# Performance work log

Hardware: AMD Instinct MI355X
Metric: run time of the kernel (lower is better)

## Reference

```python
import jax, jax.numpy as jnp
import numpy as np

B, T, INPUT_DIM = 32, 256, 512
VQ_DIM = 128
NUM_EMBED = 8192
CODEBOOK_NUM = 1
SPLIT_NUM = 4
FREQ = INPUT_DIM // 2 + 1  # 257


def setup_inputs() -> dict:
    key = jax.random.key(0)
    k1, k2, k3, k4 = jax.random.split(key, 4)
    x = jax.random.normal(k1, (B, T, INPUT_DIM), dtype=jnp.float32)
    # xavier_normal_ on (input_dim, vq_dim): std = sqrt(2/(fan_in+fan_out))
    xav_std = float(np.sqrt(2.0 / (INPUT_DIM + VQ_DIM)))
    projector = jax.random.normal(k2, (INPUT_DIM, VQ_DIM), dtype=jnp.float32) * xav_std
    codebook = jax.random.normal(k3, (CODEBOOK_NUM, NUM_EMBED, VQ_DIM), dtype=jnp.float32)
    random_matrix = jax.random.randint(k4, (FREQ,), 0, SPLIT_NUM, dtype=jnp.int32)
    return {"x": x, "projector": projector, "codebook": codebook,
            "random_matrix": random_matrix}


def reference(x, projector, codebook, random_matrix):
    n = x.shape[-1]
    x_fft = jnp.fft.rfft(x, axis=-1)                              # [B,T,F] complex
    # masks[s, f] = (random_matrix[f] == s); vectorizes the per-split list
    masks = (random_matrix[None, :] == jnp.arange(SPLIT_NUM)[:, None])  # [S,F] bool
    x_sub = x_fft[:, :, None, :] * masks                           # [B,T,S,F]
    x_recon = jnp.fft.irfft(x_sub, n=n, axis=-1)                   # [B,T,S,n]
    feat = jnp.einsum('btns,sd->btnd', x_recon, projector)         # [B,T,S,D]
    feat = feat / jnp.linalg.norm(feat, axis=-1, keepdims=True)
    cb = codebook / jnp.linalg.norm(codebook, axis=-1, keepdims=True)  # [C,M,D]
    sim = jnp.einsum('btnd,cmd->btncm', feat, cb)                  # [B,T,S,C,M]
    return jnp.argmax(sim, axis=-1)                                # [B,T,S,C]
```

## Files before the change

kernel.cpp:

```cpp
#include <hip/hip_runtime.h>
#include <math.h>

#define BT 8192
#define NDIM 512
#define NFREQ 257
#define DDIM 128
#define NEMBED 8192
#define NQ 4
#define ROWS 32768

typedef _Float16 half8 __attribute__((ext_vector_type(8)));
typedef float f32x4 __attribute__((ext_vector_type(4)));

#define SCALE_DN 2.44140625e-4f

__global__ __launch_bounds__(256) void prep_kernel(const float* __restrict__ cb,
                                                   const float* __restrict__ proj,
                                                   const int* __restrict__ rm,
                                                   _Float16* __restrict__ chi,
                                                   _Float16* __restrict__ clo,
                                                   _Float16* __restrict__ Wth,
                                                   _Float16* __restrict__ Wtl) {
    int t = threadIdx.x;
    if (blockIdx.x < 512) {
        __shared__ float tile[16][132];
        __shared__ float rns[16];
        int tileIdx = blockIdx.x;
        int row = t >> 4, seg = t & 15;
        const float* src = cb + ((size_t)tileIdx * 16 + row) * DDIM + seg * 8;
        float4 v0 = *(const float4*)src;
        float4 v1 = *(const float4*)(src + 4);
        *(float4*)&tile[row][seg * 8] = v0;
        *(float4*)&tile[row][seg * 8 + 4] = v1;
        float ss = v0.x * v0.x;
        ss = fmaf(v0.y, v0.y, ss); ss = fmaf(v0.z, v0.z, ss); ss = fmaf(v0.w, v0.w, ss);
        ss = fmaf(v1.x, v1.x, ss); ss = fmaf(v1.y, v1.y, ss);
        ss = fmaf(v1.z, v1.z, ss); ss = fmaf(v1.w, v1.w, ss);
#pragma unroll
        for (int m = 1; m < 16; m <<= 1) ss += __shfl_xor(ss, m);
        if (seg == 0) rns[row] = 1.0f / sqrtf(ss);
        __syncthreads();
        int cr = t & 15, lgq = (t >> 4) & 3, kt = t >> 6;
        int k0 = kt * 32 + lgq * 8;
        float rn = rns[cr];
        half8 oh, ol;
#pragma unroll
        for (int j = 0; j < 8; ++j) {
            float f = tile[cr][k0 + j] * rn;
            _Float16 h = (_Float16)f;
            oh[j] = h;
            ol[j] = (_Float16)((f - (float)h) * 4096.0f);
        }
        size_t dst = (size_t)tileIdx * 2048 + t * 8;
        *(half8*)(chi + dst) = oh;
        *(half8*)(clo + dst) = ol;
    } else {
        __shared__ float ctab[512];
        __shared__ float Ks[512];
        __shared__ int rms[NFREQ];
        int bxp = blockIdx.x - 512;
        int s = bxp & 3, ntp = bxp >> 2;
        int d = t & 127;
        int n0 = ntp * 16 + (t >> 7) * 8;
        for (int i = t; i < 512; i += 256) ctab[i] = cospif((float)i * (1.0f / 256.0f));
        for (int i = t; i < NFREQ; i += 256) rms[i] = rm[i];
        __syncthreads();
        for (int base = t; base < 512; base += 256) {
            float acc = 0.0f;
            for (int f = 0; f < NFREQ; ++f) {
                float w = (f == 0 || f == 256) ? 1.0f : 2.0f;
                float c = w * ctab[(f * base) & 511];
                acc += (rms[f] == s) ? c : 0.0f;
            }
            Ks[base] = acc * (1.0f / 512.0f);
        }
        __syncthreads();
        float acc[8] = {};
        for (int p16 = 0; p16 < 512; p16 += 16) {
            float wv[23];
#pragma unroll
            for (int j2 = 0; j2 < 23; ++j2) wv[j2] = Ks[(p16 - n0 + j2 - 7) & 511];
#pragma unroll
            for (int j = 0; j < 16; ++j) {
                float xp = proj[(p16 + j) * DDIM + d];
#pragma unroll
                for (int i = 0; i < 8; ++i)
                    acc[i] = fmaf(xp, wv[7 + j - i], acc[i]);
            }
        }
        size_t cbase = (size_t)(s * DDIM + d) * 512 + n0;
#pragma unroll
        for (int i = 0; i < 8; ++i) {
            float f = acc[i] * 256.0f;
            _Float16 h = (_Float16)f;
            Wth[cbase + i] = h;
            Wtl[cbase + i] = (_Float16)((f - (float)h) * 4096.0f);
        }
    }
}

__global__ __launch_bounds__(256) void fused_feat(const float* __restrict__ x,
                                                  const _Float16* __restrict__ Wth,
                                                  const _Float16* __restrict__ Wtl,
                                                  _Float16* __restrict__ fhi,
                                                  _Float16* __restrict__ flo) {
    __shared__ __align__(16) char smem[59392];
    float* xs = (float*)smem;
    _Float16* Wh = (_Float16*)(smem + 18432);
    _Float16* Wl = (_Float16*)(smem + 38912);

    int t = threadIdx.x;
    int w = t >> 6, lr = t & 15, lg = (t >> 4) & 3;
    int row0 = blockIdx.x * 64;
    int sIdx = blockIdx.y;

    int xr_r = t >> 2, xr_c = (t & 3) * 8;
    int wcol = t >> 1, wh_h = t & 1;
    const float* xsrc = x + (size_t)(row0 + xr_r) * NDIM + xr_c;
    const _Float16* whsrc = Wth + (size_t)(sIdx * 128 + wcol) * 512 + wh_h * 16;
    const _Float16* wlsrc = Wtl + (size_t)(sIdx * 128 + wcol) * 512 + wh_h * 16;

    f32x4 c0[8], c1[8];
#pragma unroll
    for (int i = 0; i < 8; ++i) { c0[i] = (f32x4){0.f,0.f,0.f,0.f}; c1[i] = c0[i]; }

    {
        float4 a0 = *(const float4*)(xsrc);
        float4 a1 = *(const float4*)(xsrc + 4);
        *(float4*)&xs[xr_r * 36 + xr_c] = a0;
        *(float4*)&xs[xr_r * 36 + xr_c + 4] = a1;
        half8 h0 = *(const half8*)(whsrc);
        half8 h1 = *(const half8*)(whsrc + 8);
        half8 l0 = *(const half8*)(wlsrc);
        half8 l1 = *(const half8*)(wlsrc + 8);
        *(half8*)&Wh[wcol * 40 + wh_h * 16] = h0;
        *(half8*)&Wh[wcol * 40 + wh_h * 16 + 8] = h1;
        *(half8*)&Wl[wcol * 40 + wh_h * 16] = l0;
        *(half8*)&Wl[wcol * 40 + wh_h * 16 + 8] = l1;
    }

    for (int it = 0; it < 16; ++it) {
        __syncthreads();
        int buf = it & 1;
        float4 nx0, nx1; half8 nh0, nh1, nl0, nl1;
        bool have = (it + 1) < 16;
        if (have) {
            int k0 = (it + 1) * 32;
            nx0 = *(const float4*)(xsrc + k0);
            nx1 = *(const float4*)(xsrc + k0 + 4);
            nh0 = *(const half8*)(whsrc + k0);
            nh1 = *(const half8*)(whsrc + k0 + 8);
            nl0 = *(const half8*)(wlsrc + k0);
            nl1 = *(const half8*)(wlsrc + k0 + 8);
        }
        const float* xb = xs + buf * 2304;
        float4 f0 = *(const float4*)&xb[(w * 16 + lr) * 36 + lg * 8];
        float4 f1 = *(const float4*)&xb[(w * 16 + lr) * 36 + lg * 8 + 4];
        float fv[8] = {f0.x, f0.y, f0.z, f0.w, f1.x, f1.y, f1.z, f1.w};
        half8 ah, al;
#pragma unroll
        for (int j = 0; j < 8; ++j) {
            _Float16 h = (_Float16)fv[j];
            ah[j] = h;
            al[j] = (_Float16)((fv[j] - (float)h) * 4096.0f);
        }
        const _Float16* whb = Wh + buf * 5120;
        const _Float16* wlb = Wl + buf * 5120;
#pragma unroll
        for (int set = 0; set < 8; ++set) {
            int bcol = set * 16 + lr;
            half8 bh = *(const half8*)&whb[bcol * 40 + lg * 8];
            half8 bl = *(const half8*)&wlb[bcol * 40 + lg * 8];
            c0[set] = __builtin_amdgcn_mfma_f32_16x16x32_f16(ah, bh, c0[set], 0, 0, 0);
            c1[set] = __builtin_amdgcn_mfma_f32_16x16x32_f16(ah, bl, c1[set], 0, 0, 0);
            c1[set] = __builtin_amdgcn_mfma_f32_16x16x32_f16(al, bh, c1[set], 0, 0, 0);
        }
        __syncthreads();
        if (have) {
            *(float4*)&xs[(buf ^ 1) * 2304 + xr_r * 36 + xr_c] = nx0;
            *(float4*)&xs[(buf ^ 1) * 2304 + xr_r * 36 + xr_c + 4] = nx1;
            _Float16* dh = Wh + (buf ^ 1) * 5120 + wcol * 40 + wh_h * 16;
            _Float16* dl = Wl + (buf ^ 1) * 5120 + wcol * 40 + wh_h * 16;
            *(half8*)(dh) = nh0; *(half8*)(dh + 8) = nh1;
            *(half8*)(dl) = nl0; *(half8*)(dl + 8) = nl1;
        }
    }
    __syncthreads();

    float* few = (float*)smem + w * 2112;
    float ss[4] = {0.f, 0.f, 0.f, 0.f};
    float vv[8][4];
#pragma unroll
    for (int set = 0; set < 8; ++set)
#pragma unroll
        for (int r = 0; r < 4; ++r) {
            float v = fmaf(c1[set][r], SCALE_DN, c0[set][r]);
            vv[set][r] = v;
            ss[r] = fmaf(v, v, ss[r]);
        }
#pragma unroll
    for (int r = 0; r < 4; ++r) {
#pragma unroll
        for (int m = 1; m < 16; m <<= 1) ss[r] += __shfl_xor(ss[r], m);
    }
    float rn[4];
#pragma unroll
    for (int r = 0; r < 4; ++r) rn[r] = rsqrtf(ss[r]);
#pragma unroll
    for (int set = 0; set < 8; ++set)
#pragma unroll
        for (int r = 0; r < 4; ++r)
            few[(4 * lg + r) * 132 + set * 16 + lr] = vv[set][r] * rn[r];
    __syncthreads();
    int l = t & 63;
    int rr = l >> 2, q = l & 3;
    size_t btg = (size_t)(row0 + w * 16 + rr);
    size_t dst = (btg * 4 + sIdx) * DDIM + q * 32;
#pragma unroll
    for (int g = 0; g < 4; ++g) {
        half8 oh, ol;
#pragma unroll
        for (int j = 0; j < 8; ++j) {
            float f = few[rr * 132 + q * 32 + g * 8 + j];
            _Float16 h = (_Float16)f;
            oh[j] = h;
            ol[j] = (_Float16)((f - (float)h) * 4096.0f);
        }
        *(half8*)(fhi + dst + g * 8) = oh;
        *(half8*)(flo + dst + g * 8) = ol;
    }
}

__global__ __launch_bounds__(256, 2) void sim_argmax_part(const _Float16* __restrict__ fhi,
                                                          const _Float16* __restrict__ flo,
                                                          const _Float16* __restrict__ chi,
                                                          const _Float16* __restrict__ clo,
                                                          float* __restrict__ pv,
                                                          int* __restrict__ pi) {
    __shared__ float redv[256][17];
    __shared__ int   redi[256][17];

    int t = threadIdx.x;
    int w = t >> 6, l = t & 63, lr = t & 15, lg = (t >> 4) & 3;
    int row0 = blockIdx.x * 256;
    int q = blockIdx.y;

    half8 ahi[4][4], alo[4][4];
#pragma unroll
    for (int s = 0; s < 4; ++s)
#pragma unroll
        for (int kt = 0; kt < 4; ++kt) {
            size_t off = (size_t)(row0 + w * 64 + s * 16 + lr) * DDIM + kt * 32 + lg * 8;
            ahi[s][kt] = *(const half8*)(fhi + off);
            alo[s][kt] = *(const half8*)(flo + off);
        }

    const half8* cf = (const half8*)chi;
    const half8* cv = (const half8*)clo;
    size_t base = (size_t)(q * (NEMBED / NQ / 16)) * 256 + l;

    half8 bh[4], bl[4];
#pragma unroll
    for (int kt = 0; kt < 4; ++kt) {
        bh[kt] = cf[base + kt * 64];
        bl[kt] = cv[base + kt * 64];
    }

    float best[4][4];
    int btile[4][4];
#pragma unroll
    for (int s = 0; s < 4; ++s)
#pragma unroll
        for (int r = 0; r < 4; ++r) { best[s][r] = -1e30f; btile[s][r] = 0; }

    f32x4 zz = (f32x4){0.f, 0.f, 0.f, 0.f};
    f32x4 pb0_2 = zz, pb1_2 = zz, pb0_3 = zz, pb1_3 = zz;

    const int NT = NEMBED / (16 * NQ);
    for (int it = 0; it < NT; ++it) {
        f32x4 a0_0 = zz, a1_0 = zz, a0_1 = zz, a1_1 = zz;
#pragma unroll
        for (int kt = 0; kt < 4; ++kt) {
            a0_0 = __builtin_amdgcn_mfma_f32_16x16x32_f16(ahi[0][kt], bh[kt], a0_0, 0, 0, 0);
            a1_0 = __builtin_amdgcn_mfma_f32_16x16x32_f16(ahi[0][kt], bl[kt], a1_0, 0, 0, 0);
            a1_0 = __builtin_amdgcn_mfma_f32_16x16x32_f16(alo[0][kt], bh[kt], a1_0, 0, 0, 0);
            a0_1 = __builtin_amdgcn_mfma_f32_16x16x32_f16(ahi[1][kt], bh[kt], a0_1, 0, 0, 0);
            a1_1 = __builtin_amdgcn_mfma_f32_16x16x32_f16(ahi[1][kt], bl[kt], a1_1, 0, 0, 0);
            a1_1 = __builtin_amdgcn_mfma_f32_16x16x32_f16(alo[1][kt], bh[kt], a1_1, 0, 0, 0);
        }
        if (it > 0) {
#pragma unroll
            for (int r = 0; r < 4; ++r) {
                float v2 = fmaf(pb1_2[r], SCALE_DN, pb0_2[r]);
                if (v2 > best[2][r]) { best[2][r] = v2; btile[2][r] = it - 1; }
                float v3 = fmaf(pb1_3[r], SCALE_DN, pb0_3[r]);
                if (v3 > best[3][r]) { best[3][r] = v3; btile[3][r] = it - 1; }
            }
        }
        pb0_2 = zz; pb1_2 = zz; pb0_3 = zz; pb1_3 = zz;
        size_t nb = base + (size_t)(it + 1) * 256;
        bool have = (it + 1) < NT;
#pragma unroll
        for (int kt = 0; kt < 4; ++kt) {
            pb0_2 = __builtin_amdgcn_mfma_f32_16x16x32_f16(ahi[2][kt], bh[kt], pb0_2, 0, 0, 0);
            pb1_2 = __builtin_amdgcn_mfma_f32_16x16x32_f16(ahi[2][kt], bl[kt], pb1_2, 0, 0, 0);
            pb1_2 = __builtin_amdgcn_mfma_f32_16x16x32_f16(alo[2][kt], bh[kt], pb1_2, 0, 0, 0);
            pb0_3 = __builtin_amdgcn_mfma_f32_16x16x32_f16(ahi[3][kt], bh[kt], pb0_3, 0, 0, 0);
            pb1_3 = __builtin_amdgcn_mfma_f32_16x16x32_f16(ahi[3][kt], bl[kt], pb1_3, 0, 0, 0);
            pb1_3 = __builtin_amdgcn_mfma_f32_16x16x32_f16(alo[3][kt], bh[kt], pb1_3, 0, 0, 0);
            if (have) {
                bh[kt] = cf[nb + kt * 64];
                bl[kt] = cv[nb + kt * 64];
            }
        }
#pragma unroll
        for (int r = 0; r < 4; ++r) {
            float v0 = fmaf(a1_0[r], SCALE_DN, a0_0[r]);
            if (v0 > best[0][r]) { best[0][r] = v0; btile[0][r] = it; }
            float v1 = fmaf(a1_1[r], SCALE_DN, a0_1[r]);
            if (v1 > best[1][r]) { best[1][r] = v1; btile[1][r] = it; }
        }
    }
#pragma unroll
    for (int r = 0; r < 4; ++r) {
        float v2 = fmaf(pb1_2[r], SCALE_DN, pb0_2[r]);
        if (v2 > best[2][r]) { best[2][r] = v2; btile[2][r] = NT - 1; }
        float v3 = fmaf(pb1_3[r], SCALE_DN, pb0_3[r]);
        if (v3 > best[3][r]) { best[3][r] = v3; btile[3][r] = NT - 1; }
    }

#pragma unroll
    for (int s = 0; s < 4; ++s)
#pragma unroll
        for (int r = 0; r < 4; ++r) {
            int row = w * 64 + s * 16 + 4 * lg + r;
            redv[row][lr] = best[s][r];
            redi[row][lr] = q * (NEMBED / NQ) + btile[s][r] * 16 + lr;
        }
    __syncthreads();
    {
        float bv = redv[t][0]; int bi = redi[t][0];
#pragma unroll
        for (int c = 1; c < 16; ++c) {
            float v = redv[t][c]; int ii = redi[t][c];
            if (v > bv || (v == bv && ii < bi)) { bv = v; bi = ii; }
        }
        pv[(size_t)q * ROWS + row0 + t] = bv;
        pi[(size_t)q * ROWS + row0 + t] = bi;
    }
}

__global__ __launch_bounds__(256) void merge_argmax(const float* __restrict__ pv,
                                                    const int* __restrict__ pi,
                                                    int* __restrict__ out) {
    int row = blockIdx.x * 256 + threadIdx.x;
    float bv = pv[row]; int bi = pi[row];
#pragma unroll
    for (int q = 1; q < NQ; ++q) {
        float v = pv[(size_t)q * ROWS + row];
        if (v > bv) { bv = v; bi = pi[(size_t)q * ROWS + row]; }
    }
    out[row] = bi;
}

extern "C" void kernel_launch(void* const* d_in, const int* in_sizes, int n_in,
                              void* d_out, int out_size, void* d_ws, size_t ws_size,
                              hipStream_t stream) {
    const float* x    = (const float*)d_in[0];
    const float* proj = (const float*)d_in[1];
    const float* cb   = (const float*)d_in[2];
    const int*   rm   = (const int*)d_in[3];
    int* out = (int*)d_out;

    char* wsb = (char*)d_ws;
    _Float16* Wth  = (_Float16*)(wsb + 0);
    _Float16* Wtl  = (_Float16*)(wsb + 524288);
    _Float16* chi  = (_Float16*)(wsb + 1048576);
    _Float16* clo  = (_Float16*)(wsb + 3145728);
    _Float16* fhi  = (_Float16*)(wsb + 5242880);
    _Float16* flo  = (_Float16*)(wsb + 13631488);
    float*    pv   = (float*)(wsb + 22020096);
    int*      pi   = (int*)(wsb + 22544384);

    prep_kernel<<<640, 256, 0, stream>>>(cb, proj, rm, chi, clo, Wth, Wtl);
    fused_feat<<<dim3(128, 4), 256, 0, stream>>>(x, Wth, Wtl, fhi, flo);
    sim_argmax_part<<<dim3(ROWS / 256, NQ), 256, 0, stream>>>(fhi, flo, chi, clo, pv, pi);
    merge_argmax<<<ROWS / 256, 256, 0, stream>>>(pv, pi, out);
}
```

Measured before the change: 287.5 us.

## Pre-swizzle projector weights into MFMA fragment layout and drop LDS staging

The prep kernel now writes the combined projector weights in a layout that matches the MFMA B-fragment order, so fused_feat loads B fragments and x rows straight from global memory. This removes the LDS double buffer and its barriers. The sim_argmax kernel also drops the software-pipelined split of subtiles and instead issues all four subtiles' MFMAs together inside s_setprio raised priority. The changes aim to cut LDS traffic and synchronisation, but they rely on cache hits for the repeated global loads and give up the overlap between MFMA work and argmax updates.

```diff
diff --git a/kernel.cpp b/kernel.cpp
--- a/kernel.cpp
+++ b/kernel.cpp
@@ -88,14 +88,19 @@
                     acc[i] = fmaf(xp, wv[7 + j - i], acc[i]);
             }
         }
-        size_t cbase = (size_t)(s * DDIM + d) * 512 + n0;
+        int set = d >> 4, lr = d & 15;
+        int itk = n0 >> 5, lg = (n0 >> 3) & 3;
+        size_t idx8 = ((size_t)((s * 16 + itk) * 8 + set)) * 64 + lg * 16 + lr;
+        half8 oh, ol;
 #pragma unroll
         for (int i = 0; i < 8; ++i) {
             float f = acc[i] * 256.0f;
             _Float16 h = (_Float16)f;
-            Wth[cbase + i] = h;
-            Wtl[cbase + i] = (_Float16)((f - (float)h) * 4096.0f);
-        }
+            oh[i] = h;
+            ol[i] = (_Float16)((f - (float)h) * 4096.0f);
+        }
+        *(half8*)(Wth + idx8 * 8) = oh;
+        *(half8*)(Wtl + idx8 * 8) = ol;
     }
 }
 
@@ -104,58 +109,24 @@
                                                   const _Float16* __restrict__ Wtl,
                                                   _Float16* __restrict__ fhi,
                                                   _Float16* __restrict__ flo) {
-    __shared__ __align__(16) char smem[59392];
-    float* xs = (float*)smem;
-    _Float16* Wh = (_Float16*)(smem + 18432);
-    _Float16* Wl = (_Float16*)(smem + 38912);
+    __shared__ float few[4][16][132];
 
     int t = threadIdx.x;
     int w = t >> 6, lr = t & 15, lg = (t >> 4) & 3;
     int row0 = blockIdx.x * 64;
     int sIdx = blockIdx.y;
 
-    int xr_r = t >> 2, xr_c = (t & 3) * 8;
-    int wcol = t >> 1, wh_h = t & 1;
-    const float* xsrc = x + (size_t)(row0 + xr_r) * NDIM + xr_c;
-    const _Float16* whsrc = Wth + (size_t)(sIdx * 128 + wcol) * 512 + wh_h * 16;
-    const _Float16* wlsrc = Wtl + (size_t)(sIdx * 128 + wcol) * 512 + wh_h * 16;
+    const half8* wh = (const half8*)Wth;
+    const half8* wl = (const half8*)Wtl;
+    const float* xrow = x + (size_t)(row0 + w * 16 + lr) * NDIM + lg * 8;
 
     f32x4 c0[8], c1[8];
 #pragma unroll
     for (int i = 0; i < 8; ++i) { c0[i] = (f32x4){0.f,0.f,0.f,0.f}; c1[i] = c0[i]; }
 
-    {
-        float4 a0 = *(const float4*)(xsrc);
-        float4 a1 = *(const float4*)(xsrc + 4);
-        *(float4*)&xs[xr_r * 36 + xr_c] = a0;
-        *(float4*)&xs[xr_r * 36 + xr_c + 4] = a1;
-        half8 h0 = *(const half8*)(whsrc);
-        half8 h1 = *(const half8*)(whsrc + 8);
-        half8 l0 = *(const half8*)(wlsrc);
-        half8 l1 = *(const half8*)(wlsrc + 8);
-        *(half8*)&Wh[wcol * 40 + wh_h * 16] = h0;
-        *(half8*)&Wh[wcol * 40 + wh_h * 16 + 8] = h1;
-        *(half8*)&Wl[wcol * 40 + wh_h * 16] = l0;
-        *(half8*)&Wl[wcol * 40 + wh_h * 16 + 8] = l1;
-    }
-
     for (int it = 0; it < 16; ++it) {
-        __syncthreads();
-        int buf = it & 1;
-        float4 nx0, nx1; half8 nh0, nh1, nl0, nl1;
-        bool have = (it + 1) < 16;
-        if (have) {
-            int k0 = (it + 1) * 32;
-            nx0 = *(const float4*)(xsrc + k0);
-            nx1 = *(const float4*)(xsrc + k0 + 4);
-            nh0 = *(const half8*)(whsrc + k0);
-            nh1 = *(const half8*)(whsrc + k0 + 8);
-            nl0 = *(const half8*)(wlsrc + k0);
-            nl1 = *(const half8*)(wlsrc + k0 + 8);
-        }
-        const float* xb = xs + buf * 2304;
-        float4 f0 = *(const float4*)&xb[(w * 16 + lr) * 36 + lg * 8];
-        float4 f1 = *(const float4*)&xb[(w * 16 + lr) * 36 + lg * 8 + 4];
+        float4 f0 = *(const float4*)(xrow + it * 32);
+        float4 f1 = *(const float4*)(xrow + it * 32 + 4);
         float fv[8] = {f0.x, f0.y, f0.z, f0.w, f1.x, f1.y, f1.z, f1.w};
         half8 ah, al;
 #pragma unroll
@@ -164,30 +135,17 @@
             ah[j] = h;
             al[j] = (_Float16)((fv[j] - (float)h) * 4096.0f);
         }
-        const _Float16* whb = Wh + buf * 5120;
-        const _Float16* wlb = Wl + buf * 5120;
+        size_t wb = ((size_t)(sIdx * 16 + it) * 8) * 64 + lg * 16 + lr;
 #pragma unroll
         for (int set = 0; set < 8; ++set) {
-            int bcol = set * 16 + lr;
-            half8 bh = *(const half8*)&whb[bcol * 40 + lg * 8];
-            half8 bl = *(const half8*)&wlb[bcol * 40 + lg * 8];
+            half8 bh = wh[wb + set * 64];
+            half8 bl = wl[wb + set * 64];
             c0[set] = __builtin_amdgcn_mfma_f32_16x16x32_f16(ah, bh, c0[set], 0, 0, 0);
             c1[set] = __builtin_amdgcn_mfma_f32_16x16x32_f16(ah, bl, c1[set], 0, 0, 0);
             c1[set] = __builtin_amdgcn_mfma_f32_16x16x32_f16(al, bh, c1[set], 0, 0, 0);
         }
-        __syncthreads();
-        if (have) {
-            *(float4*)&xs[(buf ^ 1) * 2304 + xr_r * 36 + xr_c] = nx0;
-            *(float4*)&xs[(buf ^ 1) * 2304 + xr_r * 36 + xr_c + 4] = nx1;
-            _Float16* dh = Wh + (buf ^ 1) * 5120 + wcol * 40 + wh_h * 16;
-            _Float16* dl = Wl + (buf ^ 1) * 5120 + wcol * 40 + wh_h * 16;
-            *(half8*)(dh) = nh0; *(half8*)(dh + 8) = nh1;
-            *(half8*)(dl) = nl0; *(half8*)(dl + 8) = nl1;
-        }
-    }
-    __syncthreads();
-
-    float* few = (float*)smem + w * 2112;
+    }
+
     float ss[4] = {0.f, 0.f, 0.f, 0.f};
     float vv[8][4];
 #pragma unroll
@@ -210,7 +168,7 @@
     for (int set = 0; set < 8; ++set)
 #pragma unroll
         for (int r = 0; r < 4; ++r)
-            few[(4 * lg + r) * 132 + set * 16 + lr] = vv[set][r] * rn[r];
+            few[w][4 * lg + r][set * 16 + lr] = vv[set][r] * rn[r];
     __syncthreads();
     int l = t & 63;
     int rr = l >> 2, q = l & 3;
@@ -221,7 +179,7 @@
         half8 oh, ol;
 #pragma unroll
         for (int j = 0; j < 8; ++j) {
-            float f = few[rr * 132 + q * 32 + g * 8 + j];
+            float f = few[w][rr][q * 32 + g * 8 + j];
             _Float16 h = (_Float16)f;
             oh[j] = h;
             ol[j] = (_Float16)((f - (float)h) * 4096.0f);
@@ -273,60 +231,35 @@
 #pragma unroll
         for (int r = 0; r < 4; ++r) { best[s][r] = -1e30f; btile[s][r] = 0; }
 
-    f32x4 zz = (f32x4){0.f, 0.f, 0.f, 0.f};
-    f32x4 pb0_2 = zz, pb1_2 = zz, pb0_3 = zz, pb1_3 = zz;
-
     const int NT = NEMBED / (16 * NQ);
     for (int it = 0; it < NT; ++it) {
-        f32x4 a0_0 = zz, a1_0 = zz, a0_1 = zz, a1_1 = zz;
-#pragma unroll
-        for (int kt = 0; kt < 4; ++kt) {
-            a0_0 = __builtin_amdgcn_mfma_f32_16x16x32_f16(ahi[0][kt], bh[kt], a0_0, 0, 0, 0);
-            a1_0 = __builtin_amdgcn_mfma_f32_16x16x32_f16(ahi[0][kt], bl[kt], a1_0, 0, 0, 0);
-            a1_0 = __builtin_amdgcn_mfma_f32_16x16x32_f16(alo[0][kt], bh[kt], a1_0, 0, 0, 0);
-            a0_1 = __builtin_amdgcn_mfma_f32_16x16x32_f16(ahi[1][kt], bh[kt], a0_1, 0, 0, 0);
-            a1_1 = __builtin_amdgcn_mfma_f32_16x16x32_f16(ahi[1][kt], bl[kt], a1_1, 0, 0, 0);
-            a1_1 = __builtin_amdgcn_mfma_f32_16x16x32_f16(alo[1][kt], bh[kt], a1_1, 0, 0, 0);
-        }
-        if (it > 0) {
-#pragma unroll
-            for (int r = 0; r < 4; ++r) {
-                float v2 = fmaf(pb1_2[r], SCALE_DN, pb0_2[r]);
-                if (v2 > best[2][r]) { best[2][r] = v2; btile[2][r] = it - 1; }
-                float v3 = fmaf(pb1_3[r], SCALE_DN, pb0_3[r]);
-                if (v3 > best[3][r]) { best[3][r] = v3; btile[3][r] = it - 1; }
-            }
-        }
-        pb0_2 = zz; pb1_2 = zz; pb0_3 = zz; pb1_3 = zz;
+        f32x4 a0[4], a1[4];
+#pragma unroll
+        for (int s = 0; s < 4; ++s) { a0[s] = (f32x4){0.f,0.f,0.f,0.f}; a1[s] = a0[s]; }
         size_t nb = base + (size_t)(it + 1) * 256;
         bool have = (it + 1) < NT;
+        __builtin_amdgcn_s_setprio(1);
 #pragma unroll
         for (int kt = 0; kt < 4; ++kt) {
-            pb0_2 = __builtin_amdgcn_mfma_f32_16x16x32_f16(ahi[2][kt], bh[kt], pb0_2, 0, 0, 0);
-            pb1_2 = __builtin_amdgcn_mfma_f32_16x16x32_f16(ahi[2][kt], bl[kt], pb1_2, 0, 0, 0);
-            pb1_2 = __builtin_amdgcn_mfma_f32_16x16x32_f16(alo[2][kt], bh[kt], pb1_2, 0, 0, 0);
-            pb0_3 = __builtin_amdgcn_mfma_f32_16x16x32_f16(ahi[3][kt], bh[kt], pb0_3, 0, 0, 0);
-            pb1_3 = __builtin_amdgcn_mfma_f32_16x16x32_f16(ahi[3][kt], bl[kt], pb1_3, 0, 0, 0);
-            pb1_3 = __builtin_amdgcn_mfma_f32_16x16x32_f16(alo[3][kt], bh[kt], pb1_3, 0, 0, 0);
+#pragma unroll
+            for (int s = 0; s < 4; ++s) {
+                a0[s] = __builtin_amdgcn_mfma_f32_16x16x32_f16(ahi[s][kt], bh[kt], a0[s], 0, 0, 0);
+                a1[s] = __builtin_amdgcn_mfma_f32_16x16x32_f16(ahi[s][kt], bl[kt], a1[s], 0, 0, 0);
+                a1[s] = __builtin_amdgcn_mfma_f32_16x16x32_f16(alo[s][kt], bh[kt], a1[s], 0, 0, 0);
+            }
             if (have) {
                 bh[kt] = cf[nb + kt * 64];
                 bl[kt] = cv[nb + kt * 64];
             }
         }
-#pragma unroll
-        for (int r = 0; r < 4; ++r) {
-            float v0 = fmaf(a1_0[r], SCALE_DN, a0_0[r]);
-            if (v0 > best[0][r]) { best[0][r] = v0; btile[0][r] = it; }
-            float v1 = fmaf(a1_1[r], SCALE_DN, a0_1[r]);
-            if (v1 > best[1][r]) { best[1][r] = v1; btile[1][r] = it; }
-        }
-    }
-#pragma unroll
-    for (int r = 0; r < 4; ++r) {
-        float v2 = fmaf(pb1_2[r], SCALE_DN, pb0_2[r]);
-        if (v2 > best[2][r]) { best[2][r] = v2; btile[2][r] = NT - 1; }
-        float v3 = fmaf(pb1_3[r], SCALE_DN, pb0_3[r]);
-        if (v3 > best[3][r]) { best[3][r] = v3; btile[3][r] = NT - 1; }
+        __builtin_amdgcn_s_setprio(0);
+#pragma unroll
+        for (int s = 0; s < 4; ++s)
+#pragma unroll
+            for (int r = 0; r < 4; ++r) {
+                float v = fmaf(a1[s][r], SCALE_DN, a0[s][r]);
+                if (v > best[s][r]) { best[s][r] = v; btile[s][r] = it; }
+            }
     }
 
 #pragma unroll
```

Result: slower. 296.7 us (+3.2%).
